# Kernel tuning notes

Hardware: AMD Instinct MI355X
Metric: run time of the kernel (lower is better)

## Reference

```python
import jax, jax.numpy as jnp
import numpy as np

N_AGENTS = 8; N_HEADS = 4; HYP = 128; EMB = 32; ENT_DIM = 64
BS = 64; T = 64; NE = 32


def setup_inputs() -> dict:
    key = jax.random.key(0)
    ks = jax.random.split(key, 8)
    p = lambda k, shape: jax.random.normal(k, shape, dtype=jnp.float32) * 0.1
    return {
        "agent_qs": jax.random.normal(ks[0], (BS, T, N_AGENTS), dtype=jnp.float32),
        "entities": jax.random.normal(ks[1], (BS, T, NE, ENT_DIM), dtype=jnp.float32),
        "entity_mask": jax.random.randint(ks[2], (BS, T, NE), 0, 2, dtype=jnp.int32),
        "fc1_w": p(ks[3], (4, HYP, ENT_DIM)), "fc1_b": jnp.zeros((4, HYP), jnp.float32),
        "qkv_w": p(ks[4], (4, 3 * HYP, HYP)), "qkv_b": jnp.zeros((4, 3 * HYP), jnp.float32),
        "out_w": p(ks[5], (4, HYP, HYP)), "out_b": jnp.zeros((4, HYP), jnp.float32),
        "fc2_w": p(ks[6], (4, EMB, HYP)), "fc2_b": jnp.zeros((4, EMB), jnp.float32),
    }


def _hypernet(entities, emask, fc1_w, fc1_b, qkv_w, qkv_b, out_w, out_b, fc2_w, fc2_b):
    # entities: [B, ne, ed]; emask: [B, ne] int (1 = entity absent)
    B, ne, _ = entities.shape
    hd = HYP // N_HEADS
    x1 = jax.nn.relu(jnp.einsum('bne,he->bnh', entities, fc1_w) + fc1_b)  # [B, ne, HYP]
    agent_mask = emask[:, :N_AGENTS]                                      # [B, na]
    # attn_mask = 1 - (1-agent_mask) x (1-entity_mask); nonzero => masked out
    attn_mask = 1.0 - (1.0 - agent_mask.astype(jnp.float32))[:, :, None] * \
                      (1.0 - emask.astype(jnp.float32))[:, None, :]       # [B, na, ne]
    qkv = jnp.einsum('bnh,gh->bng', x1, qkv_w) + qkv_b                    # [B, ne, 3*HYP]
    q, k, v = jnp.split(qkv, 3, axis=-1)
    q = q[:, :N_AGENTS].reshape(B, N_AGENTS, N_HEADS, hd).transpose(0, 2, 1, 3)
    k = k.reshape(B, ne, N_HEADS, hd).transpose(0, 2, 1, 3)
    v = v.reshape(B, ne, N_HEADS, hd).transpose(0, 2, 1, 3)
    logits = jnp.einsum('bhqd,bhkd->bhqk', q, k) / jnp.sqrt(jnp.float32(hd))
    masked = attn_mask[:, None] > 0                                       # [B, 1, na, ne]
    logits = jnp.where(masked, -1e9, logits)
    w = jax.nn.softmax(logits, axis=-1)
    # rows fully masked -> zero weights (matches nan-fill in torch impl)
    w = jnp.where(jnp.all(masked, axis=-1, keepdims=True), 0.0, w)
    attn = jnp.einsum('bhqk,bhkd->bhqd', w, v).transpose(0, 2, 1, 3).reshape(B, N_AGENTS, HYP)
    x2 = jnp.einsum('bnh,oh->bno', attn, out_w) + out_b
    x2 = jnp.where(agent_mask[:, :, None] > 0, 0.0, x2)                   # post_mask
    x3 = jnp.einsum('bnh,eh->bne', x2, fc2_w) + fc2_b
    x3 = jnp.where(agent_mask[:, :, None] > 0, 0.0, x3)                   # masked_fill
    return x3  # [B, n_agents, EMB]


def reference(agent_qs, entities, entity_mask, fc1_w, fc1_b, qkv_w, qkv_b, out_w, out_b, fc2_w, fc2_b):
    bs, t, ne, ed = entities.shape
    ents = entities.reshape(bs * t, ne, ed)
    emask = entity_mask.reshape(bs * t, ne)
    qs = agent_qs.reshape(bs * t, 1, N_AGENTS)
    # vmap over the 4 stacked hypernets (w1, b1, w_final, V)
    outs = jax.vmap(_hypernet, in_axes=(None, None, 0, 0, 0, 0, 0, 0, 0, 0))(
        ents, emask, fc1_w, fc1_b, qkv_w, qkv_b, out_w, out_b, fc2_w, fc2_b)
    w1 = jax.nn.softmax(outs[0], axis=-1)            # matrix mode: [B, na, EMB]
    b1 = outs[1].mean(axis=1)[:, None, :]            # vector mode: [B, 1, EMB]
    wf = outs[2].mean(axis=1)[:, :, None]            # vector mode: [B, EMB, 1]
    wf = jax.nn.softmax(wf, axis=-1)                 # softmax over size-1 dim (faithful)
    v = outs[3].mean(axis=(1, 2))[:, None, None]     # scalar mode: [B, 1, 1]
    hidden = jnp.einsum('bqa,bae->bqe', qs, w1) + b1
    y = jnp.einsum('bqe,bek->bqk', hidden, wf) + v
    return y.reshape(bs, t, 1)
```

## Files before the change

kernel.cpp:

```cpp
#include <hip/hip_runtime.h>
#include <math.h>

#define BPB 2
#define NBLK 2048
#define SCALE 0.17677669529663687f

typedef short short8 __attribute__((ext_vector_type(8)));
typedef float f32x4 __attribute__((ext_vector_type(4)));
typedef unsigned short ushort_t;

__device__ __forceinline__ unsigned short f2bf(float x) {
  unsigned int u = __float_as_uint(x);
  u += 0x7fffu + ((u >> 16) & 1u);
  return (unsigned short)(u >> 16);
}
__device__ __forceinline__ unsigned pk2(float a, float b) {
  return (unsigned)f2bf(a) | ((unsigned)f2bf(b) << 16);
}
__device__ __forceinline__ int tile_addr(int r, int k) {
  int g = k >> 3;
  int p = (g ^ ((r >> 1) & 3)) & 3;
  return r * 32 + p * 8 + (k & 7);
}
__device__ __forceinline__ int rm_addr(int r, int k) {
  int g = k >> 3;
  int r3 = r & 7;
  int rot = ((r3 << 2) | (r3 >> 1)) & 7;
  int p = (g & 8) | ((g & 7) ^ rot);
  return r * 128 + p * 8 + (k & 7);
}

__global__ void prep(const float* __restrict__ fc1_w, const float* __restrict__ qkv_w,
                     const float* __restrict__ qkv_b, const float* __restrict__ out_w,
                     const float* __restrict__ out_b, const float* __restrict__ fc2_w,
                     const float* __restrict__ fc2_b,
                     unsigned short* __restrict__ wbf, float* __restrict__ wsf) {
  const int blk = blockIdx.x;
  const int t = threadIdx.x;
  __shared__ float cw[128], red[256], ow2s[32];
  if (blk < 40) {
    int o = blk * 256 + t;
    const float* src;
    int dst;
    if (o < 2048) {
      int gi = o >> 10, rem = o & 1023, n = rem >> 3, kg = rem & 7;
      int g = gi ? 3 : 1;
      src = fc1_w + ((g << 7) + n) * 64 + kg * 8;
      int lane = (kg & 3) * 16 + (n & 15);
      int f = (n >> 4) * 2 + (kg >> 2);
      dst = ((gi * 16 + f) * 64 + lane) * 8;
    } else if (o < 6144) {
      int o2 = o - 2048;
      int gi = o2 >> 11, rem = o2 & 2047, n = rem >> 4, kg = rem & 15;
      int g = gi ? 3 : 1;
      src = qkv_w + ((g * 384 + 128 + n) << 7) + kg * 8;
      int lane = (kg & 3) * 16 + (n & 15);
      int f = (n >> 4) * 4 + (kg >> 2);
      dst = 16384 + ((gi * 36 + f) * 64 + lane) * 8;
    } else {
      int o2 = o - 6144;
      int gi = o2 >> 11, rem = o2 & 2047, n = rem >> 4, kg = rem & 15;
      int g = gi ? 3 : 1;
      src = qkv_w + ((g * 384 + n) << 7) + kg * 8;
      int lane = (kg & 3) * 16 + (n & 15);
      int f = (n >> 4) * 4 + (kg >> 2);
      dst = 53248 + ((gi * 32 + f) * 64 + lane) * 8;
    }
    float4 v0 = *(const float4*)src;
    float4 v1 = *(const float4*)(src + 4);
    uint4 p;
    p.x = pk2(v0.x, v0.y); p.y = pk2(v0.z, v0.w);
    p.z = pk2(v1.x, v1.y); p.w = pk2(v1.z, v1.w);
    *(uint4*)&wbf[dst] = p;
  } else {
    const int mb = blk - 40;
    const int gi = mb >> 2, hh = mb & 3;
    const int g = gi ? 3 : 1;
    {
      const float* fw = fc2_w + g * 4096;
      int h2 = t & 127, half = t >> 7;
      float s = 0.f;
      for (int e = half * 16; e < half * 16 + 16; ++e) s += fw[e * 128 + h2];
      red[t] = s;
    }
    __syncthreads();
    if (t < 128) cw[t] = red[t] + red[t + 128];
    __syncthreads();
    {
      const float* ow = out_w + g * 16384;
      int hp = hh * 32 + (t & 31), ch = t >> 5;
      float s = 0.f;
      for (int h = ch * 16; h < ch * 16 + 16; ++h) s += ow[h * 128 + hp] * cw[h];
      red[t] = s;
    }
    __syncthreads();
    if (t < 32) {
      float s = 0.f;
      for (int c = 0; c < 8; ++c) s += red[c * 32 + t];
      ow2s[t] = s;
    }
    __syncthreads();
    {
      const float* qwv = qkv_w + (size_t)(g * 3 + 2) * 16384;
      int h2 = t & 127, half = t >> 7;
      float s = 0.f;
      for (int d = half * 16; d < half * 16 + 16; ++d)
        s += qwv[(hh * 32 + d) * 128 + h2] * ow2s[d];
      red[t] = s;
    }
    __syncthreads();
    if (t < 128) {
      float v = red[t] + red[t + 128];
      int k = t, kc = k >> 5, kg2 = k >> 3, j = k & 7;
      wbf[16384 + ((gi * 36 + 32 + kc) * 64 + ((kg2 & 3) * 16 + hh)) * 8 + j] = f2bf(v);
    }
    if (t < 32) red[t] = qkv_b[g * 384 + 256 + hh * 32 + t] * ow2s[t];
    __syncthreads();
    if (t < 32) {
      float s = red[t];
      for (int o = 16; o; o >>= 1) s += __shfl_xor(s, o, 32);
      if (t == 0) wsf[gi * 1024 + 512 + hh] = s;
    }
    if (hh == 0) {
      for (int idx = t; idx < 1536; idx += 256) {
        int n = 4 + (idx >> 7), k = idx & 127;
        int kc = k >> 5, kg2 = k >> 3, j = k & 7;
        wbf[16384 + ((gi * 36 + 32 + kc) * 64 + ((kg2 & 3) * 16 + n)) * 8 + j] = 0;
      }
      if (t < 128) red[t] = out_b[g * 128 + t] * cw[t] + (t < 32 ? fc2_b[g * 32 + t] : 0.f);
      __syncthreads();
      if (t < 64) {
        float s = red[t] + red[t + 64];
        for (int o = 32; o; o >>= 1) s += __shfl_xor(s, o, 64);
        if (t == 0) wsf[gi * 1024 + 516] = s;
      }
    }
  }
}

__global__ __launch_bounds__(256, 3)
void mixer(const float* __restrict__ agent_qs,
           const float* __restrict__ entities,
           const int* __restrict__ emask,
           const float* __restrict__ fc1_b,
           const float* __restrict__ qkv_b,
           const unsigned short* __restrict__ wbf,
           const float* __restrict__ wsf,
           float* __restrict__ out) {
  __shared__ __align__(16) ushort_t sE[4096];
  __shared__ __align__(16) ushort_t sX1[8192];
  __shared__ __align__(16) ushort_t sK[8192];
  __shared__ __align__(16) ushort_t sQ[2048];
  __shared__ float sVP[BPB][4][32];
  __shared__ int sMm[64];
  __shared__ float sS[4];

  const int t = threadIdx.x;
  const int lane = t & 63;
  const int w = t >> 6;
  const int r = lane & 15, kg = lane >> 4;
  const int bb0 = blockIdx.x * BPB;

  if (t < 64) sMm[t] = emask[bb0 * 32 + t];

  const short8* W1f = (const short8*)wbf;
  const short8* Wkvf = (const short8*)(wbf + 16384);
  const short8* Wqf = (const short8*)(wbf + 53248);

  {
    const float4* Eg = (const float4*)entities + (size_t)bb0 * 512;
#pragma unroll
    for (int i = 0; i < 4; ++i) {
      int f4 = i * 256 + t;
      float4 v = Eg[f4];
      int k4 = f4 & 15, e = (f4 >> 4) & 31, bbi = f4 >> 9;
      int k = k4 * 4;
      int addr = bbi * 2048 + ((e >> 4) * 2 + (k >> 5)) * 512 + tile_addr(e & 15, k & 31);
      uint2 pkv;
      pkv.x = pk2(v.x, v.y);
      pkv.y = pk2(v.z, v.w);
      *(uint2*)&sE[addr] = pkv;
    }
  }
  __syncthreads();

  float wreg[4][2][4];

  for (int gi = 0; gi < 2; ++gi) {
    const int g = gi ? 3 : 1;
    {
      const int b = w >> 1, mtl = w & 1;
      f32x4 acc[8];
#pragma unroll
      for (int nt = 0; nt < 8; ++nt) acc[nt] = {0.f, 0.f, 0.f, 0.f};
#pragma unroll
      for (int kc = 0; kc < 2; ++kc) {
        short8 ef = *(const short8*)&sE[b * 2048 + (mtl * 2 + kc) * 512 + tile_addr(r, kg * 8)];
#pragma unroll
        for (int nt = 0; nt < 8; ++nt)
          acc[nt] = __builtin_amdgcn_mfma_f32_16x16x32_bf16(
              W1f[(gi * 16 + nt * 2 + kc) * 64 + lane], ef, acc[nt], 0, 0, 0);
      }
      const float* b1 = fc1_b + g * 128;
#pragma unroll
      for (int nt = 0; nt < 8; ++nt) {
        int hbase = nt * 16 + kg * 4;
        float4 bb4 = *(const float4*)&b1[hbase];
        float v0 = fmaxf(acc[nt][0] + bb4.x, 0.f);
        float v1 = fmaxf(acc[nt][1] + bb4.y, 0.f);
        float v2 = fmaxf(acc[nt][2] + bb4.z, 0.f);
        float v3 = fmaxf(acc[nt][3] + bb4.w, 0.f);
        uint2 pkv;
        pkv.x = pk2(v0, v1);
        pkv.y = pk2(v2, v3);
        *(uint2*)&sX1[b * 4096 + (mtl * 4 + (hbase >> 5)) * 512 + tile_addr(r, hbase & 31)] = pkv;
      }
    }
    __syncthreads();
    {
      const int b = w >> 1, mtl = w & 1;
      f32x4 acc[9];
#pragma unroll
      for (int nt = 0; nt < 9; ++nt) acc[nt] = {0.f, 0.f, 0.f, 0.f};
#pragma unroll
      for (int kc = 0; kc < 4; ++kc) {
        short8 xf = *(const short8*)&sX1[b * 4096 + (mtl * 4 + kc) * 512 + tile_addr(r, kg * 8)];
#pragma unroll
        for (int nt = 0; nt < 9; ++nt)
          acc[nt] = __builtin_amdgcn_mfma_f32_16x16x32_bf16(
              Wkvf[(gi * 36 + nt * 4 + kc) * 64 + lane], xf, acc[nt], 0, 0, 0);
      }
      const float* bk = qkv_b + g * 384 + 128;
      const int ent = mtl * 16 + r;
#pragma unroll
      for (int nt = 0; nt < 8; ++nt) {
        int hbase = nt * 16 + kg * 4;
        float4 bb4 = *(const float4*)&bk[hbase];
        uint2 pkv;
        pkv.x = pk2(acc[nt][0] + bb4.x, acc[nt][1] + bb4.y);
        pkv.y = pk2(acc[nt][2] + bb4.z, acc[nt][3] + bb4.w);
        *(uint2*)&sK[b * 4096 + rm_addr(ent, hbase)] = pkv;
      }
      if (kg == 0) {
#pragma unroll
        for (int reg = 0; reg < 4; ++reg)
          sVP[b][reg][ent] = acc[8][reg] + wsf[gi * 1024 + 512 + reg];
      }
      f32x4 qacc[2];
      qacc[0] = {0.f, 0.f, 0.f, 0.f};
      qacc[1] = {0.f, 0.f, 0.f, 0.f};
      const int b_rd = r >> 3;
#pragma unroll
      for (int kc = 0; kc < 4; ++kc) {
        short8 xf = *(const short8*)&sX1[b_rd * 4096 + kc * 512 + tile_addr(r & 7, kg * 8)];
#pragma unroll
        for (int j = 0; j < 2; ++j)
          qacc[j] = __builtin_amdgcn_mfma_f32_16x16x32_bf16(
              Wqf[(gi * 32 + (w * 2 + j) * 4 + kc) * 64 + lane], xf, qacc[j], 0, 0, 0);
      }
      const float* bq = qkv_b + g * 384;
#pragma unroll
      for (int j = 0; j < 2; ++j) {
        int hbase = (w * 2 + j) * 16 + kg * 4;
        float4 bb4 = *(const float4*)&bq[hbase];
        uint2 pkv;
        pkv.x = pk2(qacc[j][0] + bb4.x, qacc[j][1] + bb4.y);
        pkv.y = pk2(qacc[j][2] + bb4.z, qacc[j][3] + bb4.w);
        *(uint2*)&sQ[(r >> 3) * 1024 + rm_addr(r & 7, hbase)] = pkv;
      }
    }
    __syncthreads();
    if (w < BPB) {
      const int b = w;
      const int cl = r;
      bool ea0 = (sMm[b * 32 + cl] == 0);
      bool ea1 = (sMm[b * 32 + 16 + cl] == 0);
      bool aa[4];
#pragma unroll
      for (int reg = 0; reg < 4; ++reg) aa[reg] = (sMm[b * 32 + ((kg * 4 + reg) & 7)] == 0);
#pragma unroll
      for (int hh = 0; hh < 4; ++hh) {
        short8 af = *(const short8*)&sQ[b * 1024 + rm_addr(lane & 7, hh * 32 + kg * 8)];
        f32x4 z = {0.f, 0.f, 0.f, 0.f};
        short8 bf0 = *(const short8*)&sK[b * 4096 + rm_addr(cl, hh * 32 + kg * 8)];
        f32x4 d0 = __builtin_amdgcn_mfma_f32_16x16x32_bf16(af, bf0, z, 0, 0, 0);
        short8 bf1 = *(const short8*)&sK[b * 4096 + rm_addr(16 + cl, hh * 32 + kg * 8)];
        f32x4 d1 = __builtin_amdgcn_mfma_f32_16x16x32_bf16(af, bf1, z, 0, 0, 0);
#pragma unroll
        for (int reg = 0; reg < 4; ++reg) {
          float lg0 = (ea0 && aa[reg]) ? d0[reg] * SCALE : -1e30f;
          float lg1 = (ea1 && aa[reg]) ? d1[reg] * SCALE : -1e30f;
          float m = fmaxf(lg0, lg1);
          for (int o = 8; o; o >>= 1) m = fmaxf(m, __shfl_xor(m, o, 16));
          float p0 = lg0 > -1e29f ? __expf(lg0 - m) : 0.f;
          float p1 = lg1 > -1e29f ? __expf(lg1 - m) : 0.f;
          float s = p0 + p1;
          for (int o = 8; o; o >>= 1) s += __shfl_xor(s, o, 16);
          float inv = s > 0.f ? 1.f / s : 0.f;
          wreg[hh][0][reg] = p0 * inv;
          wreg[hh][1][reg] = p1 * inv;
        }
      }
      float c = 0.f;
#pragma unroll
      for (int hh = 0; hh < 4; ++hh) {
        float vp0 = sVP[b][hh][cl];
        float vp1 = sVP[b][hh][16 + cl];
        float s0 = wreg[hh][0][0] + wreg[hh][0][1] + wreg[hh][0][2] + wreg[hh][0][3];
        float s1 = wreg[hh][1][0] + wreg[hh][1][1] + wreg[hh][1][2] + wreg[hh][1][3];
        c = fmaf(vp0, s0, fmaf(vp1, s1, c));
      }
      for (int o = 16; o; o >>= 1) c += __shfl_xor(c, o, 32);
      if (lane == 0) {
        int cnt = 0;
        for (int a = 0; a < 8; ++a) cnt += (sMm[b * 32 + a] == 0);
        sS[gi * 2 + b] = c + wsf[gi * 1024 + 516] * (float)cnt;
      }
    }
    __syncthreads();
  }

  if (t < BPB) {
    const float4* qs = (const float4*)(agent_qs + (size_t)(bb0 + t) * 8);
    float4 a = qs[0], b4 = qs[1];
    float q = a.x + a.y + a.z + a.w + b4.x + b4.y + b4.z + b4.w;
    out[bb0 + t] = q + sS[t] * 0.125f + sS[2 + t] * (1.f / 256.f);
  }
}

extern "C" void kernel_launch(void* const* d_in, const int* in_sizes, int n_in,
                              void* d_out, int out_size, void* d_ws, size_t ws_size,
                              hipStream_t stream) {
  const float* agent_qs = (const float*)d_in[0];
  const float* entities = (const float*)d_in[1];
  const int* emask = (const int*)d_in[2];
  const float* fc1_w = (const float*)d_in[3];
  const float* fc1_b = (const float*)d_in[4];
  const float* qkv_w = (const float*)d_in[5];
  const float* qkv_b = (const float*)d_in[6];
  const float* out_w = (const float*)d_in[7];
  const float* out_b = (const float*)d_in[8];
  const float* fc2_w = (const float*)d_in[9];
  const float* fc2_b = (const float*)d_in[10];
  float* out = (float*)d_out;
  unsigned short* wbf = (unsigned short*)d_ws;
  float* wsf = (float*)((char*)d_ws + 172032);

  prep<<<48, 256, 0, stream>>>(fc1_w, qkv_w, qkv_b, out_w, out_b, fc2_w, fc2_b, wbf, wsf);
  mixer<<<NBLK, 256, 0, stream>>>(agent_qs, entities, emask, fc1_b, qkv_b, wbf, wsf, out);
}
```

Before: 151.9 us.

## Process one batch element per wavefront with register-only shuffles instead of LDS

Each wavefront now handles a whole batch element end to end, keeping entity, X1, Q and K fragments in registers and regrouping MFMA outputs into operand layout with cross-lane shuffles rather than staging through shared memory. This removes all LDS traffic and block-wide barriers, and gives every wave attention work instead of leaving half the waves idle in the attention phase. In exchange register pressure rises sharply (occupancy hint lowered from 3 to 2), each wave loads the weight fragments independently, and many shuffle instructions are added.

```diff
diff --git a/kernel.cpp b/kernel.cpp
--- a/kernel.cpp
+++ b/kernel.cpp
@@ -1,12 +1,12 @@
 #include <hip/hip_runtime.h>
 #include <math.h>
 
-#define BPB 2
-#define NBLK 2048
+#define NBLK 1024
 #define SCALE 0.17677669529663687f
 
 typedef short short8 __attribute__((ext_vector_type(8)));
 typedef float f32x4 __attribute__((ext_vector_type(4)));
+typedef unsigned int u32x4 __attribute__((ext_vector_type(4)));
 typedef unsigned short ushort_t;
 
 __device__ __forceinline__ unsigned short f2bf(float x) {
@@ -17,17 +17,27 @@
 __device__ __forceinline__ unsigned pk2(float a, float b) {
   return (unsigned)f2bf(a) | ((unsigned)f2bf(b) << 16);
 }
+__device__ __forceinline__ short8 asfrag(u32x4 v) {
+  return __builtin_bit_cast(short8, v);
+}
 __device__ __forceinline__ int tile_addr(int r, int k) {
   int g = k >> 3;
   int p = (g ^ ((r >> 1) & 3)) & 3;
   return r * 32 + p * 8 + (k & 7);
 }
-__device__ __forceinline__ int rm_addr(int r, int k) {
-  int g = k >> 3;
-  int r3 = r & 7;
-  int rot = ((r3 << 2) | (r3 >> 1)) & 7;
-  int p = (g & 8) | ((g & 7) ^ rot);
-  return r * 128 + p * 8 + (k & 7);
+
+__device__ __forceinline__ u32x4 regroup4(unsigned p01e, unsigned p23e, unsigned p01o,
+                                          unsigned p23o, int s0, int s1, bool hi) {
+  u32x4 o;
+  int a0 = __shfl((int)p01e, s0), b0 = __shfl((int)p01o, s0);
+  int a1 = __shfl((int)p23e, s0), b1 = __shfl((int)p23o, s0);
+  int a2 = __shfl((int)p01e, s1), b2 = __shfl((int)p01o, s1);
+  int a3 = __shfl((int)p23e, s1), b3 = __shfl((int)p23o, s1);
+  o.x = (unsigned)(hi ? b0 : a0);
+  o.y = (unsigned)(hi ? b1 : a1);
+  o.z = (unsigned)(hi ? b2 : a2);
+  o.w = (unsigned)(hi ? b3 : a3);
+  return o;
 }
 
 __global__ void prep(const float* __restrict__ fc1_w, const float* __restrict__ qkv_w,
@@ -138,7 +148,7 @@
   }
 }
 
-__global__ __launch_bounds__(256, 3)
+__global__ __launch_bounds__(256, 2)
 void mixer(const float* __restrict__ agent_qs,
            const float* __restrict__ entities,
            const int* __restrict__ emask,
@@ -147,184 +157,165 @@
            const unsigned short* __restrict__ wbf,
            const float* __restrict__ wsf,
            float* __restrict__ out) {
-  __shared__ __align__(16) ushort_t sE[4096];
-  __shared__ __align__(16) ushort_t sX1[8192];
-  __shared__ __align__(16) ushort_t sK[8192];
-  __shared__ __align__(16) ushort_t sQ[2048];
-  __shared__ float sVP[BPB][4][32];
-  __shared__ int sMm[64];
-  __shared__ float sS[4];
-
   const int t = threadIdx.x;
   const int lane = t & 63;
-  const int w = t >> 6;
-  const int r = lane & 15, kg = lane >> 4;
-  const int bb0 = blockIdx.x * BPB;
-
-  if (t < 64) sMm[t] = emask[bb0 * 32 + t];
+  const int kg = lane >> 4, r = lane & 15;
+  const int b = blockIdx.x * 4 + (t >> 6);
 
   const short8* W1f = (const short8*)wbf;
   const short8* Wkvf = (const short8*)(wbf + 16384);
   const short8* Wqf = (const short8*)(wbf + 53248);
 
-  {
-    const float4* Eg = (const float4*)entities + (size_t)bb0 * 512;
-#pragma unroll
-    for (int i = 0; i < 4; ++i) {
-      int f4 = i * 256 + t;
-      float4 v = Eg[f4];
-      int k4 = f4 & 15, e = (f4 >> 4) & 31, bbi = f4 >> 9;
-      int k = k4 * 4;
-      int addr = bbi * 2048 + ((e >> 4) * 2 + (k >> 5)) * 512 + tile_addr(e & 15, k & 31);
-      uint2 pkv;
-      pkv.x = pk2(v.x, v.y);
-      pkv.y = pk2(v.z, v.w);
-      *(uint2*)&sE[addr] = pkv;
-    }
-  }
-  __syncthreads();
-
-  float wreg[4][2][4];
-
+  const int mlane = emask[b * 32 + (lane & 31)];
+  const bool me0 = __shfl(mlane, r) == 0;
+  const bool me1 = __shfl(mlane, 16 + r) == 0;
+  bool aa[4];
+#pragma unroll
+  for (int reg = 0; reg < 4; ++reg) aa[reg] = __shfl(mlane, (kg * 4 + reg) & 7) == 0;
+  const int cnt = __popcll(__ballot((lane < 8) && (mlane == 0)));
+
+  u32x4 ef[2][2];
+#pragma unroll
+  for (int mt = 0; mt < 2; ++mt)
+#pragma unroll
+    for (int kc = 0; kc < 2; ++kc) {
+      const float4* ep =
+          (const float4*)(entities + (size_t)b * 2048 + (mt * 16 + r) * 64 + kc * 32 + kg * 8);
+      float4 u0 = ep[0], u1 = ep[1];
+      u32x4 v;
+      v.x = pk2(u0.x, u0.y); v.y = pk2(u0.z, u0.w);
+      v.z = pk2(u1.x, u1.y); v.w = pk2(u1.z, u1.w);
+      ef[mt][kc] = v;
+    }
+
+  const int s0 = ((kg & 1) << 5) + r;
+  const int s1 = s0 + 16;
+  const bool hi = (kg >> 1) != 0;
+
+  float T = 0.f;
   for (int gi = 0; gi < 2; ++gi) {
     const int g = gi ? 3 : 1;
-    {
-      const int b = w >> 1, mtl = w & 1;
-      f32x4 acc[8];
-#pragma unroll
-      for (int nt = 0; nt < 8; ++nt) acc[nt] = {0.f, 0.f, 0.f, 0.f};
-#pragma unroll
-      for (int kc = 0; kc < 2; ++kc) {
-        short8 ef = *(const short8*)&sE[b * 2048 + (mtl * 2 + kc) * 512 + tile_addr(r, kg * 8)];
-#pragma unroll
-        for (int nt = 0; nt < 8; ++nt)
-          acc[nt] = __builtin_amdgcn_mfma_f32_16x16x32_bf16(
-              W1f[(gi * 16 + nt * 2 + kc) * 64 + lane], ef, acc[nt], 0, 0, 0);
-      }
-      const float* b1 = fc1_b + g * 128;
+    f32x4 ax[8][2];
+#pragma unroll
+    for (int nt = 0; nt < 8; ++nt)
+#pragma unroll
+      for (int mt = 0; mt < 2; ++mt) ax[nt][mt] = {0.f, 0.f, 0.f, 0.f};
+#pragma unroll
+    for (int kc = 0; kc < 2; ++kc)
 #pragma unroll
       for (int nt = 0; nt < 8; ++nt) {
-        int hbase = nt * 16 + kg * 4;
-        float4 bb4 = *(const float4*)&b1[hbase];
-        float v0 = fmaxf(acc[nt][0] + bb4.x, 0.f);
-        float v1 = fmaxf(acc[nt][1] + bb4.y, 0.f);
-        float v2 = fmaxf(acc[nt][2] + bb4.z, 0.f);
-        float v3 = fmaxf(acc[nt][3] + bb4.w, 0.f);
-        uint2 pkv;
-        pkv.x = pk2(v0, v1);
-        pkv.y = pk2(v2, v3);
-        *(uint2*)&sX1[b * 4096 + (mtl * 4 + (hbase >> 5)) * 512 + tile_addr(r, hbase & 31)] = pkv;
-      }
-    }
-    __syncthreads();
-    {
-      const int b = w >> 1, mtl = w & 1;
-      f32x4 acc[9];
-#pragma unroll
-      for (int nt = 0; nt < 9; ++nt) acc[nt] = {0.f, 0.f, 0.f, 0.f};
-#pragma unroll
-      for (int kc = 0; kc < 4; ++kc) {
-        short8 xf = *(const short8*)&sX1[b * 4096 + (mtl * 4 + kc) * 512 + tile_addr(r, kg * 8)];
-#pragma unroll
-        for (int nt = 0; nt < 9; ++nt)
-          acc[nt] = __builtin_amdgcn_mfma_f32_16x16x32_bf16(
-              Wkvf[(gi * 36 + nt * 4 + kc) * 64 + lane], xf, acc[nt], 0, 0, 0);
-      }
-      const float* bk = qkv_b + g * 384 + 128;
-      const int ent = mtl * 16 + r;
-#pragma unroll
-      for (int nt = 0; nt < 8; ++nt) {
-        int hbase = nt * 16 + kg * 4;
-        float4 bb4 = *(const float4*)&bk[hbase];
-        uint2 pkv;
-        pkv.x = pk2(acc[nt][0] + bb4.x, acc[nt][1] + bb4.y);
-        pkv.y = pk2(acc[nt][2] + bb4.z, acc[nt][3] + bb4.w);
-        *(uint2*)&sK[b * 4096 + rm_addr(ent, hbase)] = pkv;
-      }
-      if (kg == 0) {
-#pragma unroll
-        for (int reg = 0; reg < 4; ++reg)
-          sVP[b][reg][ent] = acc[8][reg] + wsf[gi * 1024 + 512 + reg];
-      }
-      f32x4 qacc[2];
-      qacc[0] = {0.f, 0.f, 0.f, 0.f};
-      qacc[1] = {0.f, 0.f, 0.f, 0.f};
-      const int b_rd = r >> 3;
-#pragma unroll
-      for (int kc = 0; kc < 4; ++kc) {
-        short8 xf = *(const short8*)&sX1[b_rd * 4096 + kc * 512 + tile_addr(r & 7, kg * 8)];
-#pragma unroll
-        for (int j = 0; j < 2; ++j)
-          qacc[j] = __builtin_amdgcn_mfma_f32_16x16x32_bf16(
-              Wqf[(gi * 32 + (w * 2 + j) * 4 + kc) * 64 + lane], xf, qacc[j], 0, 0, 0);
-      }
-      const float* bq = qkv_b + g * 384;
-#pragma unroll
-      for (int j = 0; j < 2; ++j) {
-        int hbase = (w * 2 + j) * 16 + kg * 4;
-        float4 bb4 = *(const float4*)&bq[hbase];
-        uint2 pkv;
-        pkv.x = pk2(qacc[j][0] + bb4.x, qacc[j][1] + bb4.y);
-        pkv.y = pk2(qacc[j][2] + bb4.z, qacc[j][3] + bb4.w);
-        *(uint2*)&sQ[(r >> 3) * 1024 + rm_addr(r & 7, hbase)] = pkv;
-      }
-    }
-    __syncthreads();
-    if (w < BPB) {
-      const int b = w;
-      const int cl = r;
-      bool ea0 = (sMm[b * 32 + cl] == 0);
-      bool ea1 = (sMm[b * 32 + 16 + cl] == 0);
-      bool aa[4];
-#pragma unroll
-      for (int reg = 0; reg < 4; ++reg) aa[reg] = (sMm[b * 32 + ((kg * 4 + reg) & 7)] == 0);
-#pragma unroll
-      for (int hh = 0; hh < 4; ++hh) {
-        short8 af = *(const short8*)&sQ[b * 1024 + rm_addr(lane & 7, hh * 32 + kg * 8)];
-        f32x4 z = {0.f, 0.f, 0.f, 0.f};
-        short8 bf0 = *(const short8*)&sK[b * 4096 + rm_addr(cl, hh * 32 + kg * 8)];
-        f32x4 d0 = __builtin_amdgcn_mfma_f32_16x16x32_bf16(af, bf0, z, 0, 0, 0);
-        short8 bf1 = *(const short8*)&sK[b * 4096 + rm_addr(16 + cl, hh * 32 + kg * 8)];
-        f32x4 d1 = __builtin_amdgcn_mfma_f32_16x16x32_bf16(af, bf1, z, 0, 0, 0);
-#pragma unroll
-        for (int reg = 0; reg < 4; ++reg) {
-          float lg0 = (ea0 && aa[reg]) ? d0[reg] * SCALE : -1e30f;
-          float lg1 = (ea1 && aa[reg]) ? d1[reg] * SCALE : -1e30f;
-          float m = fmaxf(lg0, lg1);
-          for (int o = 8; o; o >>= 1) m = fmaxf(m, __shfl_xor(m, o, 16));
-          float p0 = lg0 > -1e29f ? __expf(lg0 - m) : 0.f;
-          float p1 = lg1 > -1e29f ? __expf(lg1 - m) : 0.f;
-          float s = p0 + p1;
-          for (int o = 8; o; o >>= 1) s += __shfl_xor(s, o, 16);
-          float inv = s > 0.f ? 1.f / s : 0.f;
-          wreg[hh][0][reg] = p0 * inv;
-          wreg[hh][1][reg] = p1 * inv;
-        }
-      }
-      float c = 0.f;
-#pragma unroll
-      for (int hh = 0; hh < 4; ++hh) {
-        float vp0 = sVP[b][hh][cl];
-        float vp1 = sVP[b][hh][16 + cl];
-        float s0 = wreg[hh][0][0] + wreg[hh][0][1] + wreg[hh][0][2] + wreg[hh][0][3];
-        float s1 = wreg[hh][1][0] + wreg[hh][1][1] + wreg[hh][1][2] + wreg[hh][1][3];
-        c = fmaf(vp0, s0, fmaf(vp1, s1, c));
-      }
-      for (int o = 16; o; o >>= 1) c += __shfl_xor(c, o, 32);
-      if (lane == 0) {
-        int cnt = 0;
-        for (int a = 0; a < 8; ++a) cnt += (sMm[b * 32 + a] == 0);
-        sS[gi * 2 + b] = c + wsf[gi * 1024 + 516] * (float)cnt;
-      }
-    }
-    __syncthreads();
+        short8 wf = W1f[(gi * 16 + nt * 2 + kc) * 64 + lane];
+#pragma unroll
+        for (int mt = 0; mt < 2; ++mt)
+          ax[nt][mt] = __builtin_amdgcn_mfma_f32_16x16x32_bf16(wf, asfrag(ef[mt][kc]), ax[nt][mt], 0, 0, 0);
+      }
+    unsigned p01x[8][2], p23x[8][2];
+#pragma unroll
+    for (int nt = 0; nt < 8; ++nt) {
+      float4 b4 = *(const float4*)&fc1_b[g * 128 + nt * 16 + kg * 4];
+#pragma unroll
+      for (int mt = 0; mt < 2; ++mt) {
+        float v0 = fmaxf(ax[nt][mt][0] + b4.x, 0.f);
+        float v1 = fmaxf(ax[nt][mt][1] + b4.y, 0.f);
+        float v2 = fmaxf(ax[nt][mt][2] + b4.z, 0.f);
+        float v3 = fmaxf(ax[nt][mt][3] + b4.w, 0.f);
+        p01x[nt][mt] = pk2(v0, v1);
+        p23x[nt][mt] = pk2(v2, v3);
+      }
+    }
+    u32x4 xf[2][4];
+#pragma unroll
+    for (int mt = 0; mt < 2; ++mt)
+#pragma unroll
+      for (int c = 0; c < 4; ++c)
+        xf[mt][c] = regroup4(p01x[2 * c][mt], p23x[2 * c][mt], p01x[2 * c + 1][mt],
+                             p23x[2 * c + 1][mt], s0, s1, hi);
+    f32x4 ak[9][2];
+#pragma unroll
+    for (int nt = 0; nt < 9; ++nt)
+#pragma unroll
+      for (int mt = 0; mt < 2; ++mt) ak[nt][mt] = {0.f, 0.f, 0.f, 0.f};
+#pragma unroll
+    for (int kc = 0; kc < 4; ++kc)
+#pragma unroll
+      for (int nt = 0; nt < 9; ++nt) {
+        short8 wf = Wkvf[(gi * 36 + nt * 4 + kc) * 64 + lane];
+#pragma unroll
+        for (int mt = 0; mt < 2; ++mt)
+          ak[nt][mt] = __builtin_amdgcn_mfma_f32_16x16x32_bf16(wf, asfrag(xf[mt][kc]), ak[nt][mt], 0, 0, 0);
+      }
+    unsigned p01k[8][2], p23k[8][2];
+#pragma unroll
+    for (int nt = 0; nt < 8; ++nt) {
+      float4 b4 = *(const float4*)&qkv_b[g * 384 + 128 + nt * 16 + kg * 4];
+#pragma unroll
+      for (int mt = 0; mt < 2; ++mt) {
+        p01k[nt][mt] = pk2(ak[nt][mt][0] + b4.x, ak[nt][mt][1] + b4.y);
+        p23k[nt][mt] = pk2(ak[nt][mt][2] + b4.z, ak[nt][mt][3] + b4.w);
+      }
+    }
+    f32x4 aq[8];
+#pragma unroll
+    for (int nt = 0; nt < 8; ++nt) aq[nt] = {0.f, 0.f, 0.f, 0.f};
+#pragma unroll
+    for (int kc = 0; kc < 4; ++kc)
+#pragma unroll
+      for (int nt = 0; nt < 8; ++nt)
+        aq[nt] = __builtin_amdgcn_mfma_f32_16x16x32_bf16(
+            Wqf[(gi * 32 + nt * 4 + kc) * 64 + lane], asfrag(xf[0][kc]), aq[nt], 0, 0, 0);
+    unsigned p01q[8], p23q[8];
+#pragma unroll
+    for (int nt = 0; nt < 8; ++nt) {
+      float4 b4 = *(const float4*)&qkv_b[g * 384 + nt * 16 + kg * 4];
+      p01q[nt] = pk2(aq[nt][0] + b4.x, aq[nt][1] + b4.y);
+      p23q[nt] = pk2(aq[nt][2] + b4.z, aq[nt][3] + b4.w);
+    }
+    float c_acc = 0.f;
+#pragma unroll
+    for (int hh = 0; hh < 4; ++hh) {
+      short8 qa = asfrag(regroup4(p01q[2 * hh], p23q[2 * hh], p01q[2 * hh + 1], p23q[2 * hh + 1],
+                                  s0, s1, hi));
+      short8 kb0 = asfrag(regroup4(p01k[2 * hh][0], p23k[2 * hh][0], p01k[2 * hh + 1][0],
+                                   p23k[2 * hh + 1][0], s0, s1, hi));
+      short8 kb1 = asfrag(regroup4(p01k[2 * hh][1], p23k[2 * hh][1], p01k[2 * hh + 1][1],
+                                   p23k[2 * hh + 1][1], s0, s1, hi));
+      f32x4 z = {0.f, 0.f, 0.f, 0.f};
+      f32x4 d0 = __builtin_amdgcn_mfma_f32_16x16x32_bf16(qa, kb0, z, 0, 0, 0);
+      f32x4 d1 = __builtin_amdgcn_mfma_f32_16x16x32_bf16(qa, kb1, z, 0, 0, 0);
+      float w0[4], w1[4];
+#pragma unroll
+      for (int reg = 0; reg < 4; ++reg) {
+        float lg0 = (me0 && aa[reg]) ? d0[reg] * SCALE : -1e30f;
+        float lg1 = (me1 && aa[reg]) ? d1[reg] * SCALE : -1e30f;
+        float m = fmaxf(lg0, lg1);
+#pragma unroll
+        for (int o = 8; o; o >>= 1) m = fmaxf(m, __shfl_xor(m, o, 16));
+        float p0 = lg0 > -1e29f ? __expf(lg0 - m) : 0.f;
+        float p1 = lg1 > -1e29f ? __expf(lg1 - m) : 0.f;
+        float s = p0 + p1;
+#pragma unroll
+        for (int o = 8; o; o >>= 1) s += __shfl_xor(s, o, 16);
+        float inv = s > 0.f ? 1.f / s : 0.f;
+        w0[reg] = p0 * inv;
+        w1[reg] = p1 * inv;
+      }
+      float vb2 = wsf[gi * 1024 + 512 + hh];
+      float vp0 = __shfl(ak[8][0][hh], r) + vb2;
+      float vp1 = __shfl(ak[8][1][hh], r) + vb2;
+      float s0w = w0[0] + w0[1] + w0[2] + w0[3];
+      float s1w = w1[0] + w1[1] + w1[2] + w1[3];
+      c_acc = fmaf(vp0, s0w, fmaf(vp1, s1w, c_acc));
+    }
+#pragma unroll
+    for (int o = 16; o; o >>= 1) c_acc += __shfl_xor(c_acc, o, 32);
+    if (lane == 0)
+      T += (c_acc + wsf[gi * 1024 + 516] * (float)cnt) * (gi ? (1.f / 256.f) : 0.125f);
   }
 
-  if (t < BPB) {
-    const float4* qs = (const float4*)(agent_qs + (size_t)(bb0 + t) * 8);
+  if (lane == 0) {
+    const float4* qs = (const float4*)(agent_qs + (size_t)b * 8);
     float4 a = qs[0], b4 = qs[1];
-    float q = a.x + a.y + a.z + a.w + b4.x + b4.y + b4.z + b4.w;
-    out[bb0 + t] = q + sS[t] * 0.125f + sS[2 + t] * (1.f / 256.f);
+    out[b] = a.x + a.y + a.z + a.w + b4.x + b4.y + b4.z + b4.w + T;
   }
 }
 
```

New measurement: 187.4 us. +23.4%, slower.
